# Kernel tuning notes

Hardware: AMD Instinct MI355X
Metric: run time of the kernel (lower is better)

## Reference

```python
import jax, jax.numpy as jnp
import numpy as np

B, OBS, IMG = 16384, 256, 32
CNN_LAT, LAT, H, OUT, E = 192, 256, 256, 12, 16


def _ln(x, g, b):
    m = x.mean(-1, keepdims=True)
    v = x.var(-1, keepdims=True)
    return (x - m) / jnp.sqrt(v + 1e-5) * g + b


def _conv(x, w, b):
    y = jax.lax.conv_general_dilated(x, w, (2, 2), 'SAME',
                                     dimension_numbers=('NCHW', 'OIHW', 'NCHW'))
    return jax.nn.elu(y + b[None, :, None, None])


def setup_inputs() -> dict:
    key = jax.random.key(0)
    ks = iter(jax.random.split(key, 40))

    def lin(i, o, scale=None):
        s = (1.0 / np.sqrt(i)) if scale is None else scale
        return (jax.random.normal(next(ks), (i, o), jnp.float32) * s,
                jnp.zeros((o,), jnp.float32))

    def elin(i, o, scale=None):
        s = (1.0 / np.sqrt(i)) if scale is None else scale
        return (jax.random.normal(next(ks), (E, i, o), jnp.float32) * s,
                jnp.zeros((E, o), jnp.float32))

    inp = {}
    inp['proprio'] = jax.random.normal(next(ks), (B, OBS), jnp.float32)
    inp['camera'] = jax.random.normal(next(ks), (B, 1, IMG, IMG), jnp.float32)
    # proprioception encoder: 256 -> 128 -> 64, then LayerNorm(64)
    inp['enc_w1'], inp['enc_b1'] = lin(OBS, 128)
    inp['enc_w2'], inp['enc_b2'] = lin(128, 64)
    inp['enc_ln_g'] = jnp.ones((64,), jnp.float32)
    inp['enc_ln_b'] = jnp.zeros((64,), jnp.float32)
    # CNN: 1->16 s2, 16->32 s2, flatten 32*8*8=2048 -> 192, then LayerNorm(192)
    inp['conv1_w'] = jax.random.normal(next(ks), (16, 1, 3, 3), jnp.float32) / np.sqrt(9)
    inp['conv1_b'] = jnp.zeros((16,), jnp.float32)
    inp['conv2_w'] = jax.random.normal(next(ks), (32, 16, 3, 3), jnp.float32) / np.sqrt(16 * 9)
    inp['conv2_b'] = jnp.zeros((32,), jnp.float32)
    inp['cnn_lin_w'], inp['cnn_lin_b'] = lin(32 * 8 * 8, CNN_LAT)
    inp['cnn_ln_g'] = jnp.ones((CNN_LAT,), jnp.float32)
    inp['cnn_ln_b'] = jnp.zeros((CNN_LAT,), jnp.float32)
    # router: 256 -> 128 -> 64 -> 16 (last layer gain 0.01)
    inp['router_w1'], inp['router_b1'] = lin(LAT, 128)
    inp['router_w2'], inp['router_b2'] = lin(128, 64)
    inp['router_w3'], inp['router_b3'] = lin(64, E, 0.01)
    # 16 experts (stacked): 256 -> 256 -> 256 -> 256 -> 12 (last gain 0.01)
    inp['ew1'], inp['eb1'] = elin(LAT, H)
    inp['ew2'], inp['eb2'] = elin(H, H)
    inp['ew3'], inp['eb3'] = elin(H, H)
    inp['ew4'], inp['eb4'] = elin(H, OUT, 0.01)
    return inp


def reference(proprio, camera,
              enc_w1, enc_b1, enc_w2, enc_b2, enc_ln_g, enc_ln_b,
              conv1_w, conv1_b, conv2_w, conv2_b, cnn_lin_w, cnn_lin_b,
              cnn_ln_g, cnn_ln_b,
              router_w1, router_b1, router_w2, router_b2, router_w3, router_b3,
              ew1, eb1, ew2, eb2, ew3, eb3, ew4, eb4):
    # proprioception encoder + LayerNorm -> [B, 64]
    h = jax.nn.elu(proprio @ enc_w1 + enc_b1)
    lat1d = _ln(h @ enc_w2 + enc_b2, enc_ln_g, enc_ln_b)
    # CNN encoder -> flatten -> linear -> LayerNorm -> [B, 192]
    c = _conv(camera, conv1_w, conv1_b)          # [B,16,16,16]
    c = _conv(c, conv2_w, conv2_b)               # [B,32,8,8]
    c = c.reshape(c.shape[0], -1) @ cnn_lin_w + cnn_lin_b
    lat_cnn = _ln(c, cnn_ln_g, cnn_ln_b)
    # joint latent [B, 256]
    latent = jnp.concatenate([lat1d, lat_cnn], axis=-1)
    # router gate [B, 16]
    r = jax.nn.elu(latent @ router_w1 + router_b1)
    r = jax.nn.elu(r @ router_w2 + router_b2)
    gate = jax.nn.softmax(r @ router_w3 + router_b3, axis=-1)
    # 16 experts as grouped GEMMs: [B, E, H]
    x = jax.nn.elu(jnp.einsum('bi,eij->bej', latent, ew1) + eb1)
    x = jax.nn.elu(jnp.einsum('bej,ejk->bek', x, ew2) + eb2)
    x = jax.nn.elu(jnp.einsum('bej,ejk->bek', x, ew3) + eb3)
    expert_out = jnp.einsum('bej,ejo->beo', x, ew4) + eb4  # [B,E,OUT]
    # gate-weighted combine -> [B, OUT]
    return jnp.einsum('be,beo->bo', gate, expert_out)
```

## Files before the change

kernel.cpp:

```cpp
#include <hip/hip_runtime.h>
#include <math.h>

#define BATCH 16384
#define LATD 256
#define OUTD 12
#define NE 16

typedef short bf16x8 __attribute__((ext_vector_type(8)));
typedef float f32x4 __attribute__((ext_vector_type(4)));
typedef unsigned short u16x8 __attribute__((ext_vector_type(8)));

__device__ __forceinline__ float elu_f(float x) { return x > 0.f ? x : expm1f(x); }
__device__ __forceinline__ float elu_fast(float x) { return x > 0.f ? x : (__expf(x) - 1.f); }

__device__ __forceinline__ unsigned short f2bf(float f) {
  union { float f; unsigned int u; } a; a.f = f;
  unsigned int u = a.u;
  unsigned int r = (u + 0x7FFFu + ((u >> 16) & 1u)) >> 16;
  return (unsigned short)r;
}
__device__ __forceinline__ float bf2f(unsigned short h) {
  union { unsigned int u; float f; } a; a.u = ((unsigned int)h) << 16;
  return a.f;
}

__device__ __forceinline__ int swz(int b) { return b ^ (((b >> 9) & 7) << 4); }


__global__ __launch_bounds__(256) void k_proprio(
    const float* __restrict__ P,
    const float* __restrict__ W1, const float* __restrict__ B1,
    const float* __restrict__ W2, const float* __restrict__ B2,
    const float* __restrict__ G, const float* __restrict__ Bn,
    unsigned short* __restrict__ lat16) {
  __shared__ __align__(16) float a[32][256];
  __shared__ float h[32][128];
  __shared__ float d[32][64];
  __shared__ float mrow[32], irow[32];
  const int t = threadIdx.x;
  const size_t row0 = (size_t)blockIdx.x * 32;
  {
    const float4* s = (const float4*)(P + row0 * 256);
    float4* dd = (float4*)&a[0][0];
    #pragma unroll
    for (int i = 0; i < 8; i++) dd[t + i * 256] = s[t + i * 256];
  }
  __syncthreads();
  {
    const int c = t & 127, g0 = (t >> 7) * 16;
    float acc[16];
    #pragma unroll
    for (int i = 0; i < 16; i++) acc[i] = 0.f;
    for (int k = 0; k < 256; k++) {
      const float w = W1[k * 128 + c];
      #pragma unroll
      for (int i = 0; i < 16; i++) acc[i] += a[g0 + i][k] * w;
    }
    const float bb = B1[c];
    #pragma unroll
    for (int i = 0; i < 16; i++) h[g0 + i][c] = elu_f(acc[i] + bb);
  }
  __syncthreads();
  {
    const int c = t & 63, g0 = (t >> 6) * 8;
    float acc[8];
    #pragma unroll
    for (int i = 0; i < 8; i++) acc[i] = 0.f;
    for (int k = 0; k < 128; k++) {
      const float w = W2[k * 64 + c];
      #pragma unroll
      for (int i = 0; i < 8; i++) acc[i] += h[g0 + i][k] * w;
    }
    const float bb = B2[c];
    #pragma unroll
    for (int i = 0; i < 8; i++) d[g0 + i][c] = acc[i] + bb;
  }
  __syncthreads();
  if (t < 32) {
    float m = 0.f;
    for (int j = 0; j < 64; j++) m += d[t][j];
    m *= (1.f / 64.f);
    float v = 0.f;
    for (int j = 0; j < 64; j++) { float x = d[t][j] - m; v += x * x; }
    v *= (1.f / 64.f);
    mrow[t] = m; irow[t] = 1.f / sqrtf(v + 1e-5f);
  }
  __syncthreads();
  {
    const int r = t >> 3, ch = t & 7;
    const size_t grow = row0 + r;
    const size_t rb = grow >> 7;
    const int loc = (int)(grow & 127);
    u16x8 o;
    #pragma unroll
    for (int q = 0; q < 8; q++) {
      const int c = ch * 8 + q;
      o[q] = f2bf((d[r][c] - mrow[r]) * irow[r] * G[c] + Bn[c]);
    }
    *(u16x8*)((char*)lat16 + rb * 65536 + swz(loc * 512 + ch * 16)) = o;
  }
}

__global__ __launch_bounds__(256) void k_w2c(
    const float* __restrict__ C2W, unsigned short* __restrict__ w2g) {
  const int t = threadIdx.x;
  const int co = t >> 3, ci0 = t & 7;
  #pragma unroll
  for (int hh = 0; hh < 2; hh++) {
    const int ci = ci0 + hh * 8;
    #pragma unroll
    for (int tap = 0; tap < 16; tap++) {
      w2g[co * 256 + ci * 16 + tap] =
          (tap < 9) ? f2bf(C2W[co * 144 + ci * 9 + tap]) : (unsigned short)0;
    }
  }
}

__global__ __launch_bounds__(256) void k_conv(
    const float* __restrict__ cam,
    const float* __restrict__ C1W, const float* __restrict__ C1B,
    const unsigned short* __restrict__ w2g, const float* __restrict__ C2B,
    unsigned short* __restrict__ flat) {
  __shared__ __align__(16) float img[32 * 36];
  __shared__ float w1s[144];
  __shared__ __align__(16) unsigned short c1[16 * 17 * 20];
  __shared__ __align__(16) unsigned short Bm[64 * 256];
  __shared__ __align__(16) unsigned short obuf[2048];
  const int t = threadIdx.x;
  const int lane = t & 63, w = t >> 6;
  const int lr = lane & 15, lg = lane >> 4;
  const size_t b = blockIdx.x;
  char* c1b = (char*)c1;
  char* bmb = (char*)Bm;
  {
    const float* ip = cam + b * 1024;
    for (int i = t; i < 1024; i += 256) img[(i >> 5) * 36 + (i & 31)] = ip[i];
    if (t < 32) *(float4*)&img[t * 36 + 32] = make_float4(0.f, 0.f, 0.f, 0.f);
    if (t < 144) w1s[t] = C1W[t];
    if (t < 80) *(ushort4*)(c1b + (t / 5) * 680 + 640 + (t % 5) * 8) = make_ushort4(0, 0, 0, 0);
  }
  __syncthreads();
  {
    const int c = t >> 4, y = t & 15;
    float acc[16];
    #pragma unroll
    for (int x = 0; x < 16; x++) acc[x] = 0.f;
    #pragma unroll
    for (int dy = 0; dy < 3; dy++) {
      const int row = 2 * y + dy;
      if (row < 32) {
        float4 f4[9];
        #pragma unroll
        for (int i = 0; i < 9; i++) f4[i] = *(const float4*)&img[row * 36 + 4 * i];
        const float* rr = (const float*)f4;
        const float wa = w1s[c * 9 + dy * 3], wb = w1s[c * 9 + dy * 3 + 1], wc = w1s[c * 9 + dy * 3 + 2];
        #pragma unroll
        for (int x = 0; x < 16; x++) acc[x] += wa * rr[2 * x] + wb * rr[2 * x + 1] + wc * rr[2 * x + 2];
      }
    }
    const float bb = C1B[c];
    #pragma unroll
    for (int p = 0; p < 4; p++) {
      ushort4 v;
      v.x = f2bf(elu_fast(acc[4 * p + 0] + bb));
      v.y = f2bf(elu_fast(acc[4 * p + 1] + bb));
      v.z = f2bf(elu_fast(acc[4 * p + 2] + bb));
      v.w = f2bf(elu_fast(acc[4 * p + 3] + bb));
      *(ushort4*)(c1b + c * 680 + y * 40 + p * 8) = v;
    }
    *(ushort4*)(c1b + c * 680 + y * 40 + 32) = make_ushort4(0, 0, 0, 0);
  }
  __syncthreads();
  {
    #pragma unroll
    for (int i = 0; i < 4; i++) {
      const int item = i * 256 + t;
      const int m = item & 63, ci = item >> 6;
      const int y = m >> 3, x = m & 7;
      unsigned int pr[3]; unsigned short th[3];
      #pragma unroll
      for (int dy = 0; dy < 3; dy++) {
        const int base = ci * 680 + (2 * y + dy) * 40 + 4 * x;
        pr[dy] = *(const unsigned int*)(c1b + base);
        th[dy] = *(const unsigned short*)(c1b + base + 4);
      }
      uint4 u0;
      u0.x = pr[0];
      u0.y = ((unsigned int)th[0]) | (((unsigned int)(pr[1] & 0xFFFFu)) << 16);
      u0.z = (pr[1] >> 16) | (((unsigned int)th[1]) << 16);
      u0.w = pr[2];
      uint4 u1;
      u1.x = (unsigned int)th[2];
      u1.y = 0; u1.z = 0; u1.w = 0;
      const int bb0 = m * 512 + ci * 32;
      *(uint4*)(bmb + swz(bb0)) = u0;
      *(uint4*)(bmb + swz(bb0 + 16)) = u1;
    }
  }
  __syncthreads();
  {
    f32x4 acc[2];
    acc[0] = (f32x4){0.f, 0.f, 0.f, 0.f};
    acc[1] = (f32x4){0.f, 0.f, 0.f, 0.f};
    const int mbase = (w * 16 + lr) * 512 + lg * 16;
    #pragma unroll
    for (int ks = 0; ks < 8; ks++) {
      const bf16x8 bfr = *(const bf16x8*)(bmb + swz(mbase + ks * 64));
      #pragma unroll
      for (int nt = 0; nt < 2; nt++) {
        const bf16x8 af = *(const bf16x8*)(w2g + (nt * 16 + lr) * 256 + ks * 32 + lg * 8);
        acc[nt] = __builtin_amdgcn_mfma_f32_16x16x32_bf16(af, bfr, acc[nt], 0, 0, 0);
      }
    }
    #pragma unroll
    for (int nt = 0; nt < 2; nt++) {
      const float4 bb = *(const float4*)(C2B + nt * 16 + 4 * lg);
      const float bv[4] = { bb.x, bb.y, bb.z, bb.w };
      #pragma unroll
      for (int q = 0; q < 4; q++) {
        const int co = nt * 16 + 4 * lg + q;
        obuf[co * 64 + w * 16 + lr] = f2bf(elu_fast(acc[nt][q] + bv[q]));
      }
    }
  }
  __syncthreads();
  *(u16x8*)(flat + b * 2048 + t * 8) = *(const u16x8*)(obuf + t * 8);
}

__global__ __launch_bounds__(256) void k_cnnw(
    const float* __restrict__ W, unsigned short* __restrict__ Wb) {
  __shared__ float tile[64][65];
  const int t = threadIdx.x;
  const int k0 = blockIdx.x * 64, j0 = blockIdx.y * 64;
  for (int idx = t; idx < 4096; idx += 256) {
    const int kk = idx >> 6, jj = idx & 63;
    tile[kk][jj] = W[(size_t)(k0 + kk) * 192 + j0 + jj];
  }
  __syncthreads();
  for (int idx = t; idx < 4096; idx += 256) {
    const int jj = idx >> 6, kk = idx & 63;
    Wb[(size_t)(j0 + jj) * 2048 + k0 + kk] = f2bf(tile[kk][jj]);
  }
}

__global__ __launch_bounds__(256) void k_cnnlin(
    const unsigned short* __restrict__ Xc, const unsigned short* __restrict__ Wb,
    const float* __restrict__ bias, const float* __restrict__ G,
    const float* __restrict__ Bn, unsigned short* __restrict__ lat16, int row_base) {
  __shared__ __align__(16) unsigned short XS[32 * 256];
  __shared__ __align__(16) float Yl[32 * 196];
  __shared__ float mrow[32], irow[32];
  char* xsb = (char*)XS;
  const int t = threadIdx.x;
  const int lane = t & 63, w = t >> 6;
  const int lr = lane & 15, lg = lane >> 4;
  const int b0 = blockIdx.x * 32;
  const int j0w = w * 48;

  f32x4 acc[3][2];
  #pragma unroll
  for (int jt = 0; jt < 3; jt++)
    #pragma unroll
    for (int mt = 0; mt < 2; mt++) acc[jt][mt] = (f32x4){0.f, 0.f, 0.f, 0.f};

  for (int kc = 0; kc < 8; kc++) {
    #pragma unroll
    for (int i = 0; i < 4; i++) {
      const int f = t + i * 256;
      const int m = f >> 5;
      const int kof = (f & 31) * 8;
      const u16x8 v = *(const u16x8*)(Xc + (size_t)(b0 + m) * 2048 + kc * 256 + kof);
      *(u16x8*)(xsb + swz(m * 512 + kof * 2)) = v;
    }
    __syncthreads();
    #pragma unroll
    for (int ks = 0; ks < 8; ks++) {
      bf16x8 af[3], bfr[2];
      #pragma unroll
      for (int jt = 0; jt < 3; jt++)
        af[jt] = *(const bf16x8*)(Wb + (size_t)(j0w + jt * 16 + lr) * 2048 + kc * 256 + ks * 32 + lg * 8);
      #pragma unroll
      for (int mt = 0; mt < 2; mt++)
        bfr[mt] = *(const bf16x8*)(xsb + swz((mt * 16 + lr) * 512 + lg * 16 + ks * 64));
      #pragma unroll
      for (int jt = 0; jt < 3; jt++)
        #pragma unroll
        for (int mt = 0; mt < 2; mt++)
          acc[jt][mt] = __builtin_amdgcn_mfma_f32_16x16x32_bf16(af[jt], bfr[mt], acc[jt][mt], 0, 0, 0);
    }
    __syncthreads();
  }
  #pragma unroll
  for (int jt = 0; jt < 3; jt++) {
    const int j0 = j0w + jt * 16 + 4 * lg;
    const float4 bb = *(const float4*)(bias + j0);
    #pragma unroll
    for (int mt = 0; mt < 2; mt++) {
      const int m = mt * 16 + lr;
      f32x4 v = acc[jt][mt];
      v[0] += bb.x; v[1] += bb.y; v[2] += bb.z; v[3] += bb.w;
      *(f32x4*)&Yl[m * 196 + j0] = v;
    }
  }
  __syncthreads();
  if (t < 32) {
    float m = 0.f;
    for (int q = 0; q < 48; q++) {
      const f32x4 v = *(const f32x4*)&Yl[t * 196 + q * 4];
      m += v[0] + v[1] + v[2] + v[3];
    }
    m *= (1.f / 192.f);
    float var = 0.f;
    for (int q = 0; q < 48; q++) {
      const f32x4 v = *(const f32x4*)&Yl[t * 196 + q * 4];
      #pragma unroll
      for (int z = 0; z < 4; z++) { const float x = v[z] - m; var += x * x; }
    }
    var *= (1.f / 192.f);
    mrow[t] = m; irow[t] = 1.f / sqrtf(var + 1e-5f);
  }
  __syncthreads();
  {
    #pragma unroll
    for (int i = 0; i < 3; i++) {
      const int item = t + i * 256;
      const int m = item / 24, cq = item % 24;
      const float mm = mrow[m], iv = irow[m];
      u16x8 o;
      #pragma unroll
      for (int q = 0; q < 8; q++) {
        const int j = cq * 8 + q;
        o[q] = f2bf((Yl[m * 196 + j] - mm) * iv * G[j] + Bn[j]);
      }
      const size_t grow = (size_t)(row_base + b0 + m);
      const size_t rb = grow >> 7;
      const int loc = (int)(grow & 127);
      *(u16x8*)((char*)lat16 + rb * 65536 + swz(loc * 512 + 128 + cq * 16)) = o;
    }
  }
}

__global__ __launch_bounds__(256) void k_router(
    const unsigned short* __restrict__ lat16,
    const float* __restrict__ W1, const float* __restrict__ B1,
    const float* __restrict__ W2, const float* __restrict__ B2,
    const float* __restrict__ W3, const float* __restrict__ B3,
    float* __restrict__ gate) {
  __shared__ __align__(16) float a[32][256];
  __shared__ float h1[32][128];
  __shared__ float h2[32][64];
  __shared__ float lg[32][16];
  const int t = threadIdx.x;
  const size_t row0 = (size_t)blockIdx.x * 32;
  {
    #pragma unroll
    for (int i = 0; i < 4; i++) {
      const int cc = t + i * 256;
      const int r = cc >> 5, kc = cc & 31;
      const size_t grow = row0 + r;
      const size_t rb = grow >> 7;
      const int loc = (int)(grow & 127);
      const u16x8 h = *(const u16x8*)((const char*)lat16 + rb * 65536 + swz(loc * 512 + kc * 16));
      #pragma unroll
      for (int q = 0; q < 8; q++) a[r][kc * 8 + q] = bf2f(h[q]);
    }
  }
  __syncthreads();
  {
    const int c = t & 127, g0 = (t >> 7) * 16;
    float acc[16];
    #pragma unroll
    for (int i = 0; i < 16; i++) acc[i] = 0.f;
    for (int k = 0; k < 256; k++) {
      const float w = W1[k * 128 + c];
      #pragma unroll
      for (int i = 0; i < 16; i++) acc[i] += a[g0 + i][k] * w;
    }
    const float bb = B1[c];
    #pragma unroll
    for (int i = 0; i < 16; i++) h1[g0 + i][c] = elu_f(acc[i] + bb);
  }
  __syncthreads();
  {
    const int c = t & 63, g0 = (t >> 6) * 8;
    float acc[8];
    #pragma unroll
    for (int i = 0; i < 8; i++) acc[i] = 0.f;
    for (int k = 0; k < 128; k++) {
      const float w = W2[k * 64 + c];
      #pragma unroll
      for (int i = 0; i < 8; i++) acc[i] += h1[g0 + i][k] * w;
    }
    const float bb = B2[c];
    #pragma unroll
    for (int i = 0; i < 8; i++) h2[g0 + i][c] = elu_f(acc[i] + bb);
  }
  __syncthreads();
  for (int o = t; o < 512; o += 256) {
    const int r = o >> 4, c = o & 15;
    float acc = 0.f;
    for (int k = 0; k < 64; k++) acc += h2[r][k] * W3[k * 16 + c];
    lg[r][c] = acc + B3[c];
  }
  __syncthreads();
  if (t < 32) {
    float m = lg[t][0];
    for (int c = 1; c < 16; c++) m = fmaxf(m, lg[t][c]);
    float s = 0.f;
    float ex[16];
    for (int c = 0; c < 16; c++) { ex[c] = expf(lg[t][c] - m); s += ex[c]; }
    const float inv = 1.f / s;
    for (int c = 0; c < 16; c++) gate[(row0 + t) * 16 + c] = ex[c] * inv;
  }
}

__global__ __launch_bounds__(256) void k_wt(
    const float* __restrict__ ew1, const float* __restrict__ ew2, const float* __restrict__ ew3,
    unsigned short* __restrict__ wt1, unsigned short* __restrict__ wt2, unsigned short* __restrict__ wt3) {
  __shared__ float tile[64][65];
  const int t = threadIdx.x;
  const int zl = blockIdx.z;
  const int layer = zl >> 4, e = zl & 15;
  const float* src = (layer == 0 ? ew1 : layer == 1 ? ew2 : ew3) + (size_t)e * 65536;
  unsigned short* dst = (layer == 0 ? wt1 : layer == 1 ? wt2 : wt3) + (size_t)e * 65536;
  const int k0 = blockIdx.x * 64, j0 = blockIdx.y * 64;
  for (int idx = t; idx < 4096; idx += 256) {
    const int kk = idx >> 6, jj = idx & 63;
    tile[kk][jj] = src[(size_t)(k0 + kk) * 256 + j0 + jj];
  }
  __syncthreads();
  for (int idx = t; idx < 4096; idx += 256) {
    const int jj = idx >> 6, kk = idx & 63;
    dst[(size_t)(j0 + jj) * 256 + k0 + kk] = f2bf(tile[kk][jj]);
  }
}

__global__ __launch_bounds__(256) void k_w4t(
    const float* __restrict__ ew4, unsigned short* __restrict__ w4t) {
  const int e = blockIdx.x, k = threadIdx.x;
  #pragma unroll
  for (int j = 0; j < 16; j++) {
    const float v = (j < 12) ? ew4[(size_t)e * 3072 + k * 12 + j] : 0.f;
    w4t[(size_t)e * 4096 + j * 256 + k] = f2bf(v);
  }
}

__global__ __launch_bounds__(256, 2) void k_experts(
    const unsigned short* __restrict__ lat16, const float* __restrict__ gate,
    const unsigned short* __restrict__ wt1, const unsigned short* __restrict__ wt2,
    const unsigned short* __restrict__ wt3, const unsigned short* __restrict__ w4t,
    const float* __restrict__ EB1, const float* __restrict__ EB2,
    const float* __restrict__ EB3, const float* __restrict__ EB4,
    float* __restrict__ eout) {
  __shared__ __align__(16) unsigned short Xa[64 * 256];
  __shared__ __align__(16) unsigned short Xb[64 * 256];
  char* sa = (char*)Xa;
  char* sb = (char*)Xb;
  const int t = threadIdx.x;
  const int lane = t & 63, w = t >> 6;
  const int lr = lane & 15, lg = lane >> 4;
  const int bid = blockIdx.x;
  const int xcd = bid & 7, l = bid >> 3;
  const int e = l >> 5;
  const int rb = xcd * 32 + (l & 31);
  const int row0 = rb * 64;

  const float gv = gate[(size_t)(row0 + w * 16 + lr) * 16 + e];

  {
    const uint4* s = (const uint4*)(lat16 + (size_t)(rb >> 1) * 32768 + (size_t)(rb & 1) * 16384);
    uint4* dd = (uint4*)Xa;
    #pragma unroll
    for (int i = 0; i < 8; i++) dd[t + i * 256] = s[t + i * 256];
  }
  __syncthreads();

  const unsigned short* Wl[3] = {
    wt1 + (size_t)e * 65536, wt2 + (size_t)e * 65536, wt3 + (size_t)e * 65536 };
  const float* Bl[3] = { EB1 + e * 256, EB2 + e * 256, EB3 + e * 256 };
  const int wjb = w * 64;

  int mtb[4];
  #pragma unroll
  for (int mt = 0; mt < 4; mt++) mtb[mt] = (mt * 16 + lr) * 512 + lg * 16;

  #pragma unroll
  for (int lyr = 0; lyr < 3; lyr++) {
    const unsigned short* W = Wl[lyr];
    const char* src = (lyr & 1) ? sb : sa;
    char* dst = (lyr & 1) ? sa : sb;
    f32x4 acc[4][4];
    #pragma unroll
    for (int jt = 0; jt < 4; jt++)
      #pragma unroll
      for (int mt = 0; mt < 4; mt++) acc[jt][mt] = (f32x4){0.f, 0.f, 0.f, 0.f};
    const size_t wlane = (size_t)(wjb + lr) * 256 + lg * 8;
    for (int ks = 0; ks < 8; ks++) {
      bf16x8 af[4], bfr[4];
      #pragma unroll
      for (int jt = 0; jt < 4; jt++)
        af[jt] = *(const bf16x8*)(W + wlane + jt * 4096 + ks * 32);
      #pragma unroll
      for (int mt = 0; mt < 4; mt++)
        bfr[mt] = *(const bf16x8*)(src + swz(mtb[mt] + ks * 64));
      __builtin_amdgcn_s_setprio(1);
      #pragma unroll
      for (int jt = 0; jt < 4; jt++)
        #pragma unroll
        for (int mt = 0; mt < 4; mt++)
          acc[jt][mt] = __builtin_amdgcn_mfma_f32_16x16x32_bf16(af[jt], bfr[mt], acc[jt][mt], 0, 0, 0);
      __builtin_amdgcn_s_setprio(0);
    }
    const float* B = Bl[lyr];
    #pragma unroll
    for (int jt = 0; jt < 4; jt++) {
      const int j0 = wjb + jt * 16 + 4 * lg;
      const float4 bb = *(const float4*)(B + j0);
      #pragma unroll
      for (int mt = 0; mt < 4; mt++) {
        const int m = mt * 16 + lr;
        ushort4 h;
        h.x = f2bf(elu_fast(acc[jt][mt][0] + bb.x));
        h.y = f2bf(elu_fast(acc[jt][mt][1] + bb.y));
        h.z = f2bf(elu_fast(acc[jt][mt][2] + bb.z));
        h.w = f2bf(elu_fast(acc[jt][mt][3] + bb.w));
        *(ushort4*)(dst + swz(m * 512 + j0 * 2)) = h;
      }
    }
    __syncthreads();
  }

  {
    const unsigned short* W4 = w4t + (size_t)e * 4096;
    f32x4 a4 = (f32x4){0.f, 0.f, 0.f, 0.f};
    const size_t wl4 = (size_t)lr * 256 + lg * 8;
    const int mb = (w * 16 + lr) * 512 + lg * 16;
    #pragma unroll
    for (int ks = 0; ks < 8; ks++) {
      const bf16x8 a = *(const bf16x8*)(W4 + wl4 + ks * 32);
      const bf16x8 bv = *(const bf16x8*)(sb + swz(mb + ks * 64));
      a4 = __builtin_amdgcn_mfma_f32_16x16x32_bf16(a, bv, a4, 0, 0, 0);
    }
    const int row = row0 + w * 16 + lr;
    if (lg < 3) {
      const float4 bb = *(const float4*)(EB4 + e * 12 + 4 * lg);
      float4 o;
      o.x = gv * (a4[0] + bb.x);
      o.y = gv * (a4[1] + bb.y);
      o.z = gv * (a4[2] + bb.z);
      o.w = gv * (a4[3] + bb.w);
      *(float4*)(eout + ((size_t)e * BATCH + row) * 12 + 4 * lg) = o;
    }
  }
}

__global__ __launch_bounds__(256) void k_reduce(
    const float* __restrict__ eout, float* __restrict__ out) {
  const int i = blockIdx.x * 256 + threadIdx.x;
  if (i < BATCH * OUTD) {
    float s = 0.f;
    #pragma unroll
    for (int e = 0; e < NE; e++) s += eout[(size_t)e * (BATCH * OUTD) + i];
    out[i] = s;
  }
}

extern "C" void kernel_launch(void* const* d_in, const int* in_sizes, int n_in,
                              void* d_out, int out_size, void* d_ws, size_t ws_size,
                              hipStream_t stream) {
  (void)in_sizes; (void)n_in; (void)out_size; (void)ws_size;
  const float* proprio   = (const float*)d_in[0];
  const float* camera    = (const float*)d_in[1];
  const float* enc_w1    = (const float*)d_in[2];
  const float* enc_b1    = (const float*)d_in[3];
  const float* enc_w2    = (const float*)d_in[4];
  const float* enc_b2    = (const float*)d_in[5];
  const float* enc_ln_g  = (const float*)d_in[6];
  const float* enc_ln_b  = (const float*)d_in[7];
  const float* conv1_w   = (const float*)d_in[8];
  const float* conv1_b   = (const float*)d_in[9];
  const float* conv2_w   = (const float*)d_in[10];
  const float* conv2_b   = (const float*)d_in[11];
  const float* cnn_lin_w = (const float*)d_in[12];
  const float* cnn_lin_b = (const float*)d_in[13];
  const float* cnn_ln_g  = (const float*)d_in[14];
  const float* cnn_ln_b  = (const float*)d_in[15];
  const float* rw1 = (const float*)d_in[16];
  const float* rb1 = (const float*)d_in[17];
  const float* rw2 = (const float*)d_in[18];
  const float* rb2 = (const float*)d_in[19];
  const float* rw3 = (const float*)d_in[20];
  const float* rb3 = (const float*)d_in[21];
  const float* ew1 = (const float*)d_in[22];
  const float* eb1 = (const float*)d_in[23];
  const float* ew2 = (const float*)d_in[24];
  const float* eb2 = (const float*)d_in[25];
  const float* ew3 = (const float*)d_in[26];
  const float* eb3 = (const float*)d_in[27];
  const float* ew4 = (const float*)d_in[28];
  const float* eb4 = (const float*)d_in[29];
  float* out = (float*)d_out;

  unsigned short* lat16 = (unsigned short*)d_ws;
  float* gate = (float*)(lat16 + (size_t)BATCH * 256);
  float* eout = gate + (size_t)BATCH * NE;
  unsigned short* wt1 = (unsigned short*)(eout + (size_t)NE * BATCH * OUTD);
  unsigned short* wt2 = wt1 + (size_t)NE * 65536;
  unsigned short* wt3 = wt2 + (size_t)NE * 65536;
  unsigned short* w4t = wt3 + (size_t)NE * 65536;
  unsigned short* cnnWb = w4t + (size_t)NE * 4096;
  unsigned short* w2g = cnnWb + (size_t)192 * 2048;
  unsigned short* convflat = w2g + (size_t)32 * 256;

  k_wt<<<dim3(4, 4, 48), dim3(256), 0, stream>>>(ew1, ew2, ew3, wt1, wt2, wt3);
  k_w4t<<<dim3(16), dim3(256), 0, stream>>>(ew4, w4t);
  k_cnnw<<<dim3(32, 3), dim3(256), 0, stream>>>(cnn_lin_w, cnnWb);
  k_w2c<<<dim3(1), dim3(256), 0, stream>>>(conv2_w, w2g);
  k_proprio<<<dim3(512), dim3(256), 0, stream>>>(proprio, enc_w1, enc_b1, enc_w2, enc_b2,
                                                 enc_ln_g, enc_ln_b, lat16);
  for (int ch = 0; ch < 2; ch++) {
    k_conv<<<dim3(8192), dim3(256), 0, stream>>>(camera + (size_t)ch * 8192 * 1024,
                                                 conv1_w, conv1_b, w2g, conv2_b, convflat);
    k_cnnlin<<<dim3(256), dim3(256), 0, stream>>>(convflat, cnnWb, cnn_lin_b,
                                                  cnn_ln_g, cnn_ln_b, lat16, ch * 8192);
  }
  k_router<<<dim3(512), dim3(256), 0, stream>>>(lat16, rw1, rb1, rw2, rb2, rw3, rb3, gate);
  k_experts<<<dim3(4096), dim3(256), 0, stream>>>(lat16, gate, wt1, wt2, wt3, w4t,
                                                  eb1, eb2, eb3, eb4, eout);
  k_reduce<<<dim3(768), dim3(256), 0, stream>>>(eout, out);
}
```

Measured before the change: 608.3 us.

## Fuse weight prep kernels and split expert blocks across 8 waves

New measurement: 761.0 us. +25.1%, slower.

```diff
diff --git a/kernel.cpp b/kernel.cpp
--- a/kernel.cpp
+++ b/kernel.cpp
@@ -101,17 +101,58 @@
   }
 }
 
-__global__ __launch_bounds__(256) void k_w2c(
-    const float* __restrict__ C2W, unsigned short* __restrict__ w2g) {
+__global__ __launch_bounds__(256) void k_prep(
+    const float* __restrict__ ew1, const float* __restrict__ ew2, const float* __restrict__ ew3,
+    const float* __restrict__ ew4, const float* __restrict__ cnn_lin_w, const float* __restrict__ C2W,
+    unsigned short* __restrict__ wt1, unsigned short* __restrict__ wt2, unsigned short* __restrict__ wt3,
+    unsigned short* __restrict__ w4t, unsigned short* __restrict__ cnnWb, unsigned short* __restrict__ w2g) {
+  __shared__ float tile[64][65];
   const int t = threadIdx.x;
-  const int co = t >> 3, ci0 = t & 7;
-  #pragma unroll
-  for (int hh = 0; hh < 2; hh++) {
-    const int ci = ci0 + hh * 8;
-    #pragma unroll
-    for (int tap = 0; tap < 16; tap++) {
-      w2g[co * 256 + ci * 16 + tap] =
-          (tap < 9) ? f2bf(C2W[co * 144 + ci * 9 + tap]) : (unsigned short)0;
+  const int bid = blockIdx.x;
+  if (bid < 768) {
+    const int k0 = (bid & 3) * 64, j0 = ((bid >> 2) & 3) * 64;
+    const int zl = bid >> 4;
+    const int layer = zl >> 4, e = zl & 15;
+    const float* src = (layer == 0 ? ew1 : layer == 1 ? ew2 : ew3) + (size_t)e * 65536;
+    unsigned short* dst = (layer == 0 ? wt1 : layer == 1 ? wt2 : wt3) + (size_t)e * 65536;
+    for (int idx = t; idx < 4096; idx += 256) {
+      const int kk = idx >> 6, jj = idx & 63;
+      tile[kk][jj] = src[(size_t)(k0 + kk) * 256 + j0 + jj];
+    }
+    __syncthreads();
+    for (int idx = t; idx < 4096; idx += 256) {
+      const int jj = idx >> 6, kk = idx & 63;
+      dst[(size_t)(j0 + jj) * 256 + k0 + kk] = f2bf(tile[kk][jj]);
+    }
+  } else if (bid < 864) {
+    const int idx0 = bid - 768;
+    const int k0 = (idx0 & 31) * 64, j0 = (idx0 >> 5) * 64;
+    for (int idx = t; idx < 4096; idx += 256) {
+      const int kk = idx >> 6, jj = idx & 63;
+      tile[kk][jj] = cnn_lin_w[(size_t)(k0 + kk) * 192 + j0 + jj];
+    }
+    __syncthreads();
+    for (int idx = t; idx < 4096; idx += 256) {
+      const int jj = idx >> 6, kk = idx & 63;
+      cnnWb[(size_t)(j0 + jj) * 2048 + k0 + kk] = f2bf(tile[kk][jj]);
+    }
+  } else if (bid < 880) {
+    const int e = bid - 864, k = t;
+    #pragma unroll
+    for (int j = 0; j < 16; j++) {
+      const float v = (j < 12) ? ew4[(size_t)e * 3072 + k * 12 + j] : 0.f;
+      w4t[(size_t)e * 4096 + j * 256 + k] = f2bf(v);
+    }
+  } else {
+    const int co = t >> 3, ci0 = t & 7;
+    #pragma unroll
+    for (int hh = 0; hh < 2; hh++) {
+      const int ci = ci0 + hh * 8;
+      #pragma unroll
+      for (int tap = 0; tap < 16; tap++) {
+        w2g[co * 256 + ci * 16 + tap] =
+            (tap < 9) ? f2bf(C2W[co * 144 + ci * 9 + tap]) : (unsigned short)0;
+      }
     }
   }
 }
@@ -227,22 +268,6 @@
   *(u16x8*)(flat + b * 2048 + t * 8) = *(const u16x8*)(obuf + t * 8);
 }
 
-__global__ __launch_bounds__(256) void k_cnnw(
-    const float* __restrict__ W, unsigned short* __restrict__ Wb) {
-  __shared__ float tile[64][65];
-  const int t = threadIdx.x;
-  const int k0 = blockIdx.x * 64, j0 = blockIdx.y * 64;
-  for (int idx = t; idx < 4096; idx += 256) {
-    const int kk = idx >> 6, jj = idx & 63;
-    tile[kk][jj] = W[(size_t)(k0 + kk) * 192 + j0 + jj];
-  }
-  __syncthreads();
-  for (int idx = t; idx < 4096; idx += 256) {
-    const int jj = idx >> 6, kk = idx & 63;
-    Wb[(size_t)(j0 + jj) * 2048 + k0 + kk] = f2bf(tile[kk][jj]);
-  }
-}
-
 __global__ __launch_bounds__(256) void k_cnnlin(
     const unsigned short* __restrict__ Xc, const unsigned short* __restrict__ Wb,
     const float* __restrict__ bias, const float* __restrict__ G,
@@ -414,125 +439,98 @@
   }
 }
 
-__global__ __launch_bounds__(256) void k_wt(
-    const float* __restrict__ ew1, const float* __restrict__ ew2, const float* __restrict__ ew3,
-    unsigned short* __restrict__ wt1, unsigned short* __restrict__ wt2, unsigned short* __restrict__ wt3) {
-  __shared__ float tile[64][65];
-  const int t = threadIdx.x;
-  const int zl = blockIdx.z;
-  const int layer = zl >> 4, e = zl & 15;
-  const float* src = (layer == 0 ? ew1 : layer == 1 ? ew2 : ew3) + (size_t)e * 65536;
-  unsigned short* dst = (layer == 0 ? wt1 : layer == 1 ? wt2 : wt3) + (size_t)e * 65536;
-  const int k0 = blockIdx.x * 64, j0 = blockIdx.y * 64;
-  for (int idx = t; idx < 4096; idx += 256) {
-    const int kk = idx >> 6, jj = idx & 63;
-    tile[kk][jj] = src[(size_t)(k0 + kk) * 256 + j0 + jj];
-  }
-  __syncthreads();
-  for (int idx = t; idx < 4096; idx += 256) {
-    const int jj = idx >> 6, kk = idx & 63;
-    dst[(size_t)(j0 + jj) * 256 + k0 + kk] = f2bf(tile[kk][jj]);
-  }
-}
-
-__global__ __launch_bounds__(256) void k_w4t(
-    const float* __restrict__ ew4, unsigned short* __restrict__ w4t) {
-  const int e = blockIdx.x, k = threadIdx.x;
-  #pragma unroll
-  for (int j = 0; j < 16; j++) {
-    const float v = (j < 12) ? ew4[(size_t)e * 3072 + k * 12 + j] : 0.f;
-    w4t[(size_t)e * 4096 + j * 256 + k] = f2bf(v);
-  }
-}
-
-__global__ __launch_bounds__(256, 2) void k_experts(
+__global__ __launch_bounds__(512, 4) void k_experts(
     const unsigned short* __restrict__ lat16, const float* __restrict__ gate,
     const unsigned short* __restrict__ wt1, const unsigned short* __restrict__ wt2,
     const unsigned short* __restrict__ wt3, const unsigned short* __restrict__ w4t,
     const float* __restrict__ EB1, const float* __restrict__ EB2,
     const float* __restrict__ EB3, const float* __restrict__ EB4,
-    float* __restrict__ eout) {
+    float* __restrict__ eout, int e_base) {
   __shared__ __align__(16) unsigned short Xa[64 * 256];
   __shared__ __align__(16) unsigned short Xb[64 * 256];
   char* sa = (char*)Xa;
   char* sb = (char*)Xb;
   const int t = threadIdx.x;
   const int lane = t & 63, w = t >> 6;
+  const int jb = w & 3;
+  const int mh = w >> 2;
   const int lr = lane & 15, lg = lane >> 4;
   const int bid = blockIdx.x;
   const int xcd = bid & 7, l = bid >> 3;
-  const int e = l >> 5;
+  const int e = e_base + (l >> 5);
   const int rb = xcd * 32 + (l & 31);
   const int row0 = rb * 64;
 
-  const float gv = gate[(size_t)(row0 + w * 16 + lr) * 16 + e];
-
   {
     const uint4* s = (const uint4*)(lat16 + (size_t)(rb >> 1) * 32768 + (size_t)(rb & 1) * 16384);
     uint4* dd = (uint4*)Xa;
     #pragma unroll
-    for (int i = 0; i < 8; i++) dd[t + i * 256] = s[t + i * 256];
+    for (int i = 0; i < 4; i++) dd[t + i * 512] = s[t + i * 512];
   }
   __syncthreads();
 
   const unsigned short* Wl[3] = {
     wt1 + (size_t)e * 65536, wt2 + (size_t)e * 65536, wt3 + (size_t)e * 65536 };
   const float* Bl[3] = { EB1 + e * 256, EB2 + e * 256, EB3 + e * 256 };
-  const int wjb = w * 64;
-
-  int mtb[4];
+  const int wjb = jb * 64;
+
+  int mtb[2];
   #pragma unroll
-  for (int mt = 0; mt < 4; mt++) mtb[mt] = (mt * 16 + lr) * 512 + lg * 16;
+  for (int mt = 0; mt < 2; mt++) mtb[mt] = (mh * 32 + mt * 16 + lr) * 512 + lg * 16;
 
   #pragma unroll
   for (int lyr = 0; lyr < 3; lyr++) {
     const unsigned short* W = Wl[lyr];
     const char* src = (lyr & 1) ? sb : sa;
     char* dst = (lyr & 1) ? sa : sb;
-    f32x4 acc[4][4];
-    #pragma unroll
-    for (int jt = 0; jt < 4; jt++)
-      #pragma unroll
-      for (int mt = 0; mt < 4; mt++) acc[jt][mt] = (f32x4){0.f, 0.f, 0.f, 0.f};
+    const float* B = Bl[lyr];
+    f32x4 acc[4][2];
+    #pragma unroll
+    for (int jt = 0; jt < 4; jt++) {
+      const float4 bb = *(const float4*)(B + wjb + jt * 16 + 4 * lg);
+      #pragma unroll
+      for (int mt = 0; mt < 2; mt++)
+        acc[jt][mt] = (f32x4){bb.x, bb.y, bb.z, bb.w};
+    }
     const size_t wlane = (size_t)(wjb + lr) * 256 + lg * 8;
     for (int ks = 0; ks < 8; ks++) {
-      bf16x8 af[4], bfr[4];
+      bf16x8 af[4], bfr[2];
       #pragma unroll
       for (int jt = 0; jt < 4; jt++)
         af[jt] = *(const bf16x8*)(W + wlane + jt * 4096 + ks * 32);
       #pragma unroll
-      for (int mt = 0; mt < 4; mt++)
+      for (int mt = 0; mt < 2; mt++)
         bfr[mt] = *(const bf16x8*)(src + swz(mtb[mt] + ks * 64));
       __builtin_amdgcn_s_setprio(1);
       #pragma unroll
       for (int jt = 0; jt < 4; jt++)
         #pragma unroll
-        for (int mt = 0; mt < 4; mt++)
+        for (int mt = 0; mt < 2; mt++)
           acc[jt][mt] = __builtin_amdgcn_mfma_f32_16x16x32_bf16(af[jt], bfr[mt], acc[jt][mt], 0, 0, 0);
       __builtin_amdgcn_s_setprio(0);
     }
-    const float* B = Bl[lyr];
     #pragma unroll
     for (int jt = 0; jt < 4; jt++) {
       const int j0 = wjb + jt * 16 + 4 * lg;
-      const float4 bb = *(const float4*)(B + j0);
-      #pragma unroll
-      for (int mt = 0; mt < 4; mt++) {
-        const int m = mt * 16 + lr;
+      #pragma unroll
+      for (int mt = 0; mt < 2; mt++) {
+        const int m = mh * 32 + mt * 16 + lr;
         ushort4 h;
-        h.x = f2bf(elu_fast(acc[jt][mt][0] + bb.x));
-        h.y = f2bf(elu_fast(acc[jt][mt][1] + bb.y));
-        h.z = f2bf(elu_fast(acc[jt][mt][2] + bb.z));
-        h.w = f2bf(elu_fast(acc[jt][mt][3] + bb.w));
+        h.x = f2bf(elu_fast(acc[jt][mt][0]));
+        h.y = f2bf(elu_fast(acc[jt][mt][1]));
+        h.z = f2bf(elu_fast(acc[jt][mt][2]));
+        h.w = f2bf(elu_fast(acc[jt][mt][3]));
         *(ushort4*)(dst + swz(m * 512 + j0 * 2)) = h;
       }
     }
     __syncthreads();
   }
 
-  {
+  if (w < 4) {
     const unsigned short* W4 = w4t + (size_t)e * 4096;
-    f32x4 a4 = (f32x4){0.f, 0.f, 0.f, 0.f};
+    float4 b4 = make_float4(0.f, 0.f, 0.f, 0.f);
+    if (lg < 3) b4 = *(const float4*)(EB4 + e * 12 + 4 * lg);
+    f32x4 a4 = (f32x4){b4.x, b4.y, b4.z, b4.w};
     const size_t wl4 = (size_t)lr * 256 + lg * 8;
     const int mb = (w * 16 + lr) * 512 + lg * 16;
     #pragma unroll
@@ -543,12 +541,12 @@
     }
     const int row = row0 + w * 16 + lr;
     if (lg < 3) {
-      const float4 bb = *(const float4*)(EB4 + e * 12 + 4 * lg);
+      const float gv = gate[(size_t)row * 16 + e];
       float4 o;
-      o.x = gv * (a4[0] + bb.x);
-      o.y = gv * (a4[1] + bb.y);
-      o.z = gv * (a4[2] + bb.z);
-      o.w = gv * (a4[3] + bb.w);
+      o.x = gv * a4[0];
+      o.y = gv * a4[1];
+      o.z = gv * a4[2];
+      o.w = gv * a4[3];
       *(float4*)(eout + ((size_t)e * BATCH + row) * 12 + 4 * lg) = o;
     }
   }
@@ -612,10 +610,8 @@
   unsigned short* w2g = cnnWb + (size_t)192 * 2048;
   unsigned short* convflat = w2g + (size_t)32 * 256;
 
-  k_wt<<<dim3(4, 4, 48), dim3(256), 0, stream>>>(ew1, ew2, ew3, wt1, wt2, wt3);
-  k_w4t<<<dim3(16), dim3(256), 0, stream>>>(ew4, w4t);
-  k_cnnw<<<dim3(32, 3), dim3(256), 0, stream>>>(cnn_lin_w, cnnWb);
-  k_w2c<<<dim3(1), dim3(256), 0, stream>>>(conv2_w, w2g);
+  k_prep<<<dim3(881), dim3(256), 0, stream>>>(ew1, ew2, ew3, ew4, cnn_lin_w, conv2_w,
+                                              wt1, wt2, wt3, w4t, cnnWb, w2g);
   k_proprio<<<dim3(512), dim3(256), 0, stream>>>(proprio, enc_w1, enc_b1, enc_w2, enc_b2,
                                                  enc_ln_g, enc_ln_b, lat16);
   for (int ch = 0; ch < 2; ch++) {
@@ -625,7 +621,9 @@
                                                   cnn_ln_g, cnn_ln_b, lat16, ch * 8192);
   }
   k_router<<<dim3(512), dim3(256), 0, stream>>>(lat16, rw1, rb1, rw2, rb2, rw3, rb3, gate);
-  k_experts<<<dim3(4096), dim3(256), 0, stream>>>(lat16, gate, wt1, wt2, wt3, w4t,
-                                                  eb1, eb2, eb3, eb4, eout);
+  k_experts<<<dim3(2048), dim3(512), 0, stream>>>(lat16, gate, wt1, wt2, wt3, w4t,
+                                                  eb1, eb2, eb3, eb4, eout, 0);
+  k_experts<<<dim3(2048), dim3(512), 0, stream>>>(lat16, gate, wt1, wt2, wt3, w4t,
+                                                  eb1, eb2, eb3, eb4, eout, 8);
   k_reduce<<<dim3(768), dim3(256), 0, stream>>>(eout, out);
 }
```
